# Optimization experiments

Hardware: AMD Instinct MI355X
Metric: run time of the kernel (lower is better)

## Reference

```python
import jax, jax.numpy as jnp
import numpy as np
from jax import lax

B, S, IN, H, HEAD, OUT = 256, 512, 64, 1024, 128, 64


def setup_inputs() -> dict:
    key = jax.random.key(0)
    ks = jax.random.split(key, 9)
    sc = 0.05
    return {
        "x": jax.random.normal(ks[0], (B, S, IN), jnp.float32),
        "W_ih": jax.random.normal(ks[1], (4 * H, IN), jnp.float32) * sc,
        "b_ih": jax.random.normal(ks[2], (4 * H,), jnp.float32) * sc,
        "W_hh": jax.random.normal(ks[3], (4 * H, H), jnp.float32) * sc,
        "b_hh": jax.random.normal(ks[4], (4 * H,), jnp.float32) * sc,
        "W_dense": jax.random.normal(ks[5], (HEAD, H), jnp.float32) * sc,
        "b_dense": jax.random.normal(ks[6], (HEAD,), jnp.float32) * sc,
        "W_dense2": jax.random.normal(ks[7], (OUT, HEAD), jnp.float32) * sc,
        "b_dense2": jax.random.normal(ks[8], (OUT,), jnp.float32) * sc,
    }


def reference(x, W_ih, b_ih, W_hh, b_hh, W_dense, b_dense, W_dense2, b_dense2):
    batch = x.shape[0]
    hid = W_hh.shape[1]
    # Precompute input-to-gate projections for all timesteps in one big GEMM.
    # x: [B,S,IN] -> xg: [S,B,4H]
    xg = jnp.einsum("bsi,gi->sbg", x, W_ih) + b_ih + b_hh

    def step(carry, xg_t):
        h, c = carry
        gates = xg_t + h @ W_hh.T  # [B,4H]; PyTorch LSTMCell gate order i,f,g,o
        i, f, g, o = jnp.split(gates, 4, axis=-1)
        c = jax.nn.sigmoid(f) * c + jax.nn.sigmoid(i) * jnp.tanh(g)
        h = jax.nn.sigmoid(o) * jnp.tanh(c)
        pred = jax.nn.relu(h @ W_dense.T + b_dense) @ W_dense2.T + b_dense2
        return (h, c), pred

    h0 = jnp.zeros((batch, hid), x.dtype)
    c0 = jnp.zeros((batch, hid), x.dtype)
    _, out = lax.scan(step, (h0, c0), xg)  # out: [S,B,OUT]
    return jnp.swapaxes(out, 0, 1)  # [B,S,OUT]
```

## Files before the change

### kernel.cpp

```cpp
#include <hip/hip_runtime.h>

typedef _Float16 half_t;
typedef _Float16 half8 __attribute__((ext_vector_type(8)));
typedef _Float16 half4 __attribute__((ext_vector_type(4)));
typedef float float4v __attribute__((ext_vector_type(4)));

#define BB    256
#define SS    512
#define IND   64
#define HH    1024
#define HEADD 128
#define OUTD  64
#define NKT   34
#define WLDS_HALVES (4 * NKT * 512)
#define PRE_STRIDE 68
#define DP_OFF   (WLDS_HALVES * 2 + 4 * 16 * PRE_STRIDE * 4)
#define FLAG_OFF (DP_OFF + 3 * 64 * 4 * 4)
#define SMEM_BYTES (FLAG_OFF + 32)
#define BUFV (BB * HH)
#define GO_OFF   8192
#define DCNT_OFF 10240
#define SYNC_WORDS 10368

#define MFMA16(a, b, acc) __builtin_amdgcn_mfma_f32_16x16x32_f16(a, b, acc, 0, 0, 0)

__device__ half_t g_hA[(size_t)(SS + 1) * BUFV];
__device__ half_t g_dbuf[(size_t)SS * 256 * HEADD];
__device__ unsigned int g_sync[SYNC_WORDS];

__device__ __forceinline__ void astore8(half_t* p, half4 v) {
  union { half4 h; unsigned long long u; } r; r.h = v;
  __hip_atomic_store((unsigned long long*)p, r.u, __ATOMIC_RELAXED,
                     __HIP_MEMORY_SCOPE_AGENT);
}
__device__ __forceinline__ void astore2(half_t* p, half_t v) {
  union { half_t h; unsigned short u; } r; r.h = v;
  __hip_atomic_store((unsigned short*)p, r.u, __ATOMIC_RELAXED,
                     __HIP_MEMORY_SCOPE_AGENT);
}


__global__ __launch_bounds__(256) void init_state() {
  const size_t i = (size_t)blockIdx.x * 256 + threadIdx.x;
  *(unsigned long long*)(g_hA + i * 4) = 0ULL;
  if (blockIdx.x == 0)
    for (int j = threadIdx.x; j < SYNC_WORDS; j += 256) g_sync[j] = 0;
}

__global__ __launch_bounds__(256) void pack_x(const float* __restrict__ x,
                                              half_t* __restrict__ xA) {
  const int t = blockIdx.x, mt = blockIdx.y;
  const int tid = threadIdx.x;
  const int kt = tid >> 7;
  const int lane = (tid >> 1) & 63;
  const int jh = (tid & 1) * 4;
  const int row = mt * 16 + (lane & 15);
  const int k = kt * 32 + (lane >> 4) * 8 + jh;
  const float* s = x + (size_t)row * SS * IND + (size_t)t * IND + k;
  half_t* d = xA + (((size_t)t * 16 + mt) * 2 + kt) * 512 + lane * 8 + jh;
  d[0] = (half_t)s[0]; d[1] = (half_t)s[1];
  d[2] = (half_t)s[2]; d[3] = (half_t)s[3];
}

__global__ __launch_bounds__(256) void frag_pack(const float* __restrict__ src,
                                                 half_t* __restrict__ dst, int K) {
  const int cb = blockIdx.x;
  const int tid = threadIdx.x;
  const int lane = tid & 63;
  const int u = tid >> 6;
  const int nkt = K >> 5;
  const int row = cb * 16 + (lane & 15);
  for (int kt = u; kt < nkt; kt += 4) {
    const int k = kt * 32 + (lane >> 4) * 8;
    const float* s = src + (size_t)row * K + k;
    half8 h;
    #pragma unroll
    for (int j = 0; j < 8; ++j) h[j] = (half_t)s[j];
    *(half8*)(dst + ((size_t)cb * nkt + kt) * 512 + lane * 8) = h;
  }
}

__global__ __launch_bounds__(512, 2) void lstm_persistent(
    const float* __restrict__ W_hh, const float* __restrict__ W_ih,
    const float* __restrict__ b_ih, const float* __restrict__ b_hh,
    const half_t* __restrict__ xA, const half_t* __restrict__ Wd_f,
    const float* __restrict__ bd, const half_t* __restrict__ Wd2_f,
    const float* __restrict__ bd2, float* __restrict__ out) {
  extern __shared__ char smem[];
  half_t* Wlds = (half_t*)smem;
  float* pre = (float*)(smem + (size_t)WLDS_HALVES * 2);
  float* dp = (float*)(smem + DP_OFF);
  unsigned* flg = (unsigned*)(smem + FLAG_OFF);

  const int bid = blockIdx.x;
  const int xcd = bid & 7;
  const int mtile = xcd >> 1;
  const int jtile = ((bid >> 3) << 1) | (xcd & 1);
  const int j0 = jtile * 16;
  const int tid = threadIdx.x;
  const int wave = tid >> 6;
  const int lane = tid & 63;
  const int rn = lane & 15;
  const int kq = lane >> 4;

  {
    const int g = wave & 3;
    const int row = g * HH + j0 + rn;
    for (int kt = (wave >> 2); kt < NKT; kt += 2) {
      const int k = kt * 32 + kq * 8;
      const float* s = (k < HH) ? (W_hh + (size_t)row * HH + k)
                                : (W_ih + (size_t)row * IND + (k - HH));
      half8 hv;
      #pragma unroll
      for (int j = 0; j < 8; ++j) hv[j] = (half_t)s[j];
      *(half8*)(Wlds + ((size_t)g * NKT + kt) * 512 + lane * 8) = hv;
    }
  }
  if (tid < 8) flg[tid] = 0;
  __syncthreads();

  unsigned short* slotp =
      (unsigned short*)(g_sync + ((size_t)(mtile * 64 + jtile)) * 32);
  unsigned int* go_base = g_sync + GO_OFF + mtile * 512;
  const unsigned int* gop = go_base + (jtile & 15) * 32;
  unsigned int* dcnt = g_sync + DCNT_OFF + mtile * 32;

  if (wave < 4) {
    const int crow = lane >> 2;
    const int hl = (lane & 3) * 4;
    float bsum[4][4];
    #pragma unroll
    for (int g = 0; g < 4; ++g) {
      const float4v bi = *(const float4v*)(b_ih + g * HH + j0 + hl);
      const float4v bh = *(const float4v*)(b_hh + g * HH + j0 + hl);
      #pragma unroll
      for (int j = 0; j < 4; ++j) bsum[g][j] = bi[j] + bh[j];
    }
    float4v creg = {0.f, 0.f, 0.f, 0.f};

    const int mtA = mtile * 4 + wave;
    float* pw = pre + wave * (16 * PRE_STRIDE);

    const int col_s = j0 + hl;
    const int ktw = col_s >> 5;
    const int kqw = (col_s & 31) >> 3;
    const int jw = col_s & 7;
    const size_t hoff =
        (((size_t)(mtA * 32 + ktw)) * 64 + kqw * 16 + crow) * 8 + jw;

    const half_t* habase = g_hA + ((size_t)mtA * 32) * 512 + lane * 8;
    const half_t* bp = Wlds + lane * 8;
    unsigned short* myslot = slotp + wave;

    half8 breg0[8], breg1[8], breg2[8], breg3[8];
    #pragma unroll
    for (int kt = 0; kt < 8; ++kt) {
      breg0[kt] = *(const half8*)(bp + (size_t)(0 * NKT + kt) * 512);
      breg1[kt] = *(const half8*)(bp + (size_t)(1 * NKT + kt) * 512);
      breg2[kt] = *(const half8*)(bp + (size_t)(2 * NKT + kt) * 512);
      breg3[kt] = *(const half8*)(bp + (size_t)(3 * NKT + kt) * 512);
    }

    for (int t = 0; t < SS; ++t) {
      float4v a0 = {0.f, 0.f, 0.f, 0.f}, a1 = {0.f, 0.f, 0.f, 0.f};
      float4v a2 = {0.f, 0.f, 0.f, 0.f}, a3 = {0.f, 0.f, 0.f, 0.f};

      const half_t* xp = xA + (((size_t)t * 16 + mtA) * 2) * 512 + lane * 8;
      {
        const half8 xv0 = *(const half8*)xp;
        const half8 xv1 = *(const half8*)(xp + 512);
        a0 = MFMA16(xv0, *(const half8*)(bp + (size_t)(0 * NKT + 32) * 512), a0);
        a1 = MFMA16(xv0, *(const half8*)(bp + (size_t)(1 * NKT + 32) * 512), a1);
        a2 = MFMA16(xv0, *(const half8*)(bp + (size_t)(2 * NKT + 32) * 512), a2);
        a3 = MFMA16(xv0, *(const half8*)(bp + (size_t)(3 * NKT + 32) * 512), a3);
        a0 = MFMA16(xv1, *(const half8*)(bp + (size_t)(0 * NKT + 33) * 512), a0);
        a1 = MFMA16(xv1, *(const half8*)(bp + (size_t)(1 * NKT + 33) * 512), a1);
        a2 = MFMA16(xv1, *(const half8*)(bp + (size_t)(2 * NKT + 33) * 512), a2);
        a3 = MFMA16(xv1, *(const half8*)(bp + (size_t)(3 * NKT + 33) * 512), a3);
      }

      if (t >= 1) {
        const unsigned tt = (unsigned)t;
        while (__hip_atomic_load(gop, __ATOMIC_RELAXED,
                                 __HIP_MEMORY_SCOPE_AGENT) < tt)
          __builtin_amdgcn_s_sleep(1);
        asm volatile("" ::: "memory");
        if (wave == 0 && lane == 0)
          __hip_atomic_store(&flg[3], tt, __ATOMIC_RELEASE,
                             __HIP_MEMORY_SCOPE_WORKGROUP);
      }

      const half_t* ap = habase + (size_t)t * BUFV;
      #pragma unroll
      for (int kt = 0; kt < 8; ++kt) {
        const half8 av = *(const half8*)(ap + (size_t)kt * 512);
        a0 = MFMA16(av, breg0[kt], a0);
        a1 = MFMA16(av, breg1[kt], a1);
        a2 = MFMA16(av, breg2[kt], a2);
        a3 = MFMA16(av, breg3[kt], a3);
      }
      #pragma unroll 8
      for (int kt = 8; kt < 32; ++kt) {
        const half8 av = *(const half8*)(ap + (size_t)kt * 512);
        a0 = MFMA16(av, *(const half8*)(bp + (size_t)(0 * NKT + kt) * 512), a0);
        a1 = MFMA16(av, *(const half8*)(bp + (size_t)(1 * NKT + kt) * 512), a1);
        a2 = MFMA16(av, *(const half8*)(bp + (size_t)(2 * NKT + kt) * 512), a2);
        a3 = MFMA16(av, *(const half8*)(bp + (size_t)(3 * NKT + kt) * 512), a3);
      }

      #pragma unroll
      for (int r = 0; r < 4; ++r) {
        const int rl = (kq * 4 + r) * PRE_STRIDE;
        pw[rl + rn] = a0[r];
        pw[rl + 16 + rn] = a1[r];
        pw[rl + 32 + rn] = a2[r];
        pw[rl + 48 + rn] = a3[r];
      }

      const float4v pg0 = *(const float4v*)(pw + crow * PRE_STRIDE + hl);
      const float4v pg1 = *(const float4v*)(pw + crow * PRE_STRIDE + 16 + hl);
      const float4v pg2 = *(const float4v*)(pw + crow * PRE_STRIDE + 32 + hl);
      const float4v pg3 = *(const float4v*)(pw + crow * PRE_STRIDE + 48 + hl);
      half4 hnew;
      #pragma unroll
      for (int jj = 0; jj < 4; ++jj) {
        const float ig = pg0[jj] + bsum[0][jj];
        const float fg = pg1[jj] + bsum[1][jj];
        const float gg = pg2[jj] + bsum[2][jj];
        const float og = pg3[jj] + bsum[3][jj];
        const float is = 1.f / (1.f + __expf(-ig));
        const float fs = 1.f / (1.f + __expf(-fg));
        const float os = 1.f / (1.f + __expf(-og));
        const float gt = tanhf(gg);
        const float cn = fs * creg[jj] + is * gt;
        creg[jj] = cn;
        hnew[jj] = (half_t)(os * tanhf(cn));
      }
      astore8(g_hA + (size_t)(t + 1) * BUFV + hoff, hnew);

      __builtin_amdgcn_s_waitcnt(0);
      if (lane == 0)
        __hip_atomic_store(myslot, (unsigned short)(t + 1), __ATOMIC_RELAXED,
                           __HIP_MEMORY_SCOPE_AGENT);
    }

    if (wave == 0) {
      while (__hip_atomic_load(gop, __ATOMIC_RELAXED,
                               __HIP_MEMORY_SCOPE_AGENT) < (unsigned)SS)
        __builtin_amdgcn_s_sleep(1);
      asm volatile("" ::: "memory");
      if (lane == 0)
        __hip_atomic_store(&flg[3], (unsigned)SS, __ATOMIC_RELEASE,
                           __HIP_MEMORY_SCOPE_WORKGROUP);
    }

  } else if (jtile < 32) {
    const int u = wave - 4;
    const int rb = jtile >> 3, cb = jtile & 7;
    const int mt = mtile * 4 + rb;
    const half_t* hb = g_hA + ((size_t)mt * 32 + u * 8) * 512 + lane * 8;
    const half_t* bb = Wd_f + ((size_t)cb * 32 + u * 8) * 512 + lane * 8;

    for (int s = 1; s <= SS; ++s) {
      while (__hip_atomic_load(&flg[3], __ATOMIC_ACQUIRE,
                               __HIP_MEMORY_SCOPE_WORKGROUP) < (unsigned)s)
        __builtin_amdgcn_s_sleep(2);
      asm volatile("" ::: "memory");

      const half_t* ap = hb + (size_t)s * BUFV;
      float4v acc = {0.f, 0.f, 0.f, 0.f};
      #pragma unroll
      for (int kt = 0; kt < 8; ++kt)
        acc = MFMA16(*(const half8*)(ap + (size_t)kt * 512),
                     *(const half8*)(bb + (size_t)kt * 512), acc);

      if (u) {
        if (s > 1)
          while (__hip_atomic_load(&flg[4], __ATOMIC_ACQUIRE,
                                   __HIP_MEMORY_SCOPE_WORKGROUP) <
                 (unsigned)(s - 1))
            __builtin_amdgcn_s_sleep(1);
        *(float4v*)(dp + ((size_t)(u - 1) * 64 + lane) * 4) = acc;
        __hip_atomic_store(&flg[u - 1], (unsigned)s, __ATOMIC_RELEASE,
                           __HIP_MEMORY_SCOPE_WORKGROUP);
      } else {
        for (;;) {
          const unsigned f0 = __hip_atomic_load(&flg[0], __ATOMIC_ACQUIRE,
                                                __HIP_MEMORY_SCOPE_WORKGROUP);
          const unsigned f1 = __hip_atomic_load(&flg[1], __ATOMIC_ACQUIRE,
                                                __HIP_MEMORY_SCOPE_WORKGROUP);
          const unsigned f2 = __hip_atomic_load(&flg[2], __ATOMIC_ACQUIRE,
                                                __HIP_MEMORY_SCOPE_WORKGROUP);
          if (f0 >= (unsigned)s && f1 >= (unsigned)s && f2 >= (unsigned)s) break;
          __builtin_amdgcn_s_sleep(1);
        }
        asm volatile("" ::: "memory");
        #pragma unroll
        for (int i = 0; i < 3; ++i) {
          const float4v p = *(const float4v*)(dp + ((size_t)i * 64 + lane) * 4);
          #pragma unroll
          for (int r = 0; r < 4; ++r) acc[r] += p[r];
        }
        __hip_atomic_store(&flg[4], (unsigned)s, __ATOMIC_RELEASE,
                           __HIP_MEMORY_SCOPE_WORKGROUP);
        const int dcol = cb * 16 + rn;
        const float bv = bd[dcol];
        half_t* db = g_dbuf + (((size_t)(s - 1) * 16 + mt) * 16) * HEADD + dcol;
        #pragma unroll
        for (int r = 0; r < 4; ++r)
          astore2(db + (size_t)(kq * 4 + r) * HEADD,
                  (half_t)fmaxf(acc[r] + bv, 0.f));
        __builtin_amdgcn_s_waitcnt(0);
        if (lane == 0)
          __hip_atomic_fetch_add(dcnt, 1u, __ATOMIC_RELAXED,
                                 __HIP_MEMORY_SCOPE_AGENT);
      }
    }

  } else if (jtile < 48 && wave == 4) {
    const int task = jtile - 32;
    const int rb = task >> 2, cb2 = task & 3;
    const int mt = mtile * 4 + rb;
    const int m0 = mtile * 64;
    const half_t* bp2 = Wd2_f + (size_t)cb2 * 4 * 512 + lane * 8;
    for (int d = 0; d < SS; ++d) {
      if (lane == 0) {
        const unsigned tgt = 32u * (unsigned)(d + 1);
        while (__hip_atomic_load(dcnt, __ATOMIC_RELAXED,
                                 __HIP_MEMORY_SCOPE_AGENT) < tgt)
          __builtin_amdgcn_s_sleep(16);
      }
      asm volatile("" ::: "memory");
      const half_t* ap = g_dbuf + (((size_t)d * 16 + mt) * 16) * HEADD;
      float4v acc = {0.f, 0.f, 0.f, 0.f};
      #pragma unroll
      for (int kt = 0; kt < 4; ++kt) {
        const half8 af =
            *(const half8*)(ap + (size_t)rn * HEADD + kt * 32 + kq * 8);
        acc = MFMA16(af, *(const half8*)(bp2 + (size_t)kt * 512), acc);
      }
      const int ocol = cb2 * 16 + rn;
      const float bv = bd2[ocol];
      #pragma unroll
      for (int r = 0; r < 4; ++r) {
        const int row = m0 + rb * 16 + kq * 4 + r;
        out[(size_t)row * (SS * OUTD) + (size_t)d * OUTD + ocol] = acc[r] + bv;
      }
    }

  } else if (jtile == 63 && wave == 5) {
    const unsigned long long* pollp =
        (const unsigned long long*)(g_sync + ((size_t)(mtile * 64 + lane)) * 32);
    for (int t = 1; t <= SS; ++t) {
      const unsigned tt = (unsigned)t;
      for (;;) {
        const unsigned long long v = __hip_atomic_load(
            pollp, __ATOMIC_RELAXED, __HIP_MEMORY_SCOPE_AGENT);
        const unsigned f0 = (unsigned)(v & 0xffffu);
        const unsigned f1 = (unsigned)((v >> 16) & 0xffffu);
        const unsigned f2 = (unsigned)((v >> 32) & 0xffffu);
        const unsigned f3 = (unsigned)(v >> 48);
        if (__all((int)(f0 >= tt && f1 >= tt && f2 >= tt && f3 >= tt))) break;
        __builtin_amdgcn_s_sleep(1);
      }
      asm volatile("" ::: "memory");
      if (lane < 16)
        __hip_atomic_store(go_base + lane * 32, tt, __ATOMIC_RELAXED,
                           __HIP_MEMORY_SCOPE_AGENT);
    }
  }
}

extern "C" void kernel_launch(void* const* d_in, const int* in_sizes, int n_in,
                              void* d_out, int out_size, void* d_ws, size_t ws_size,
                              hipStream_t stream) {
  const float* x        = (const float*)d_in[0];
  const float* W_ih     = (const float*)d_in[1];
  const float* b_ih     = (const float*)d_in[2];
  const float* W_hh     = (const float*)d_in[3];
  const float* b_hh     = (const float*)d_in[4];
  const float* W_dense  = (const float*)d_in[5];
  const float* b_dense  = (const float*)d_in[6];
  const float* W_dense2 = (const float*)d_in[7];
  const float* b_dense2 = (const float*)d_in[8];
  float* out = (float*)d_out;

  char* p = (char*)d_ws;
  half_t* xA    = (half_t*)p; p += (size_t)SS * 16 * 1024 * 2;
  half_t* Wd_f  = (half_t*)p; p += (size_t)8 * 32 * 512 * 2;
  half_t* Wd2_f = (half_t*)p; p += (size_t)4 * 4 * 512 * 2;

  init_state<<<256, 256, 0, stream>>>();
  pack_x<<<dim3(SS, 16), 256, 0, stream>>>(x, xA);
  frag_pack<<<HEADD / 16, 256, 0, stream>>>(W_dense, Wd_f, HH);
  frag_pack<<<OUTD / 16, 256, 0, stream>>>(W_dense2, Wd2_f, HEADD);

  hipFuncSetAttribute((const void*)lstm_persistent,
                      hipFuncAttributeMaxDynamicSharedMemorySize, SMEM_BYTES);
  void* args[] = {(void*)&W_hh, (void*)&W_ih, (void*)&b_ih, (void*)&b_hh,
                  (void*)&xA, (void*)&Wd_f, (void*)&b_dense,
                  (void*)&Wd2_f, (void*)&b_dense2, (void*)&out};
  hipLaunchCooperativeKernel((void*)lstm_persistent, dim3(256), dim3(512),
                             args, SMEM_BYTES, stream);
}
```

Before: 4.263 ms.

## Replace full hidden-state history with an 8-slot ring buffer and hoist dense weights

Stores the hidden state in an 8-entry ring buffer instead of a buffer holding every timestep, so the working set stays cache-resident instead of streaming 513 full hidden-state copies through memory. To stop slots being overwritten too early, the recurrent waves now wait on the dense-stage completion counter before reusing a slot, and acquire fences replace the compiler-only barriers. The dense-head and output-stage weight fragments are also hoisted into registers. In exchange the recurrence can stall on the dense consumers, and the extra registers may reduce occupancy or cause spills.

New measurement: 9.600 ms. 2.25x slower.

```diff
diff --git a/kernel.cpp b/kernel.cpp
--- a/kernel.cpp
+++ b/kernel.cpp
@@ -18,13 +18,14 @@
 #define FLAG_OFF (DP_OFF + 3 * 64 * 4 * 4)
 #define SMEM_BYTES (FLAG_OFF + 32)
 #define BUFV (BB * HH)
+#define HRING 8
 #define GO_OFF   8192
 #define DCNT_OFF 10240
 #define SYNC_WORDS 10368
 
 #define MFMA16(a, b, acc) __builtin_amdgcn_mfma_f32_16x16x32_f16(a, b, acc, 0, 0, 0)
 
-__device__ half_t g_hA[(size_t)(SS + 1) * BUFV];
+__device__ half_t g_hA[(size_t)HRING * BUFV];
 __device__ half_t g_dbuf[(size_t)SS * 256 * HEADD];
 __device__ unsigned int g_sync[SYNC_WORDS];
 
@@ -148,7 +149,7 @@
     const size_t hoff =
         (((size_t)(mtA * 32 + ktw)) * 64 + kqw * 16 + crow) * 8 + jw;
 
-    const half_t* habase = g_hA + ((size_t)mtA * 32) * 512 + lane * 8;
+    const size_t hbase_off = ((size_t)mtA * 32) * 512 + lane * 8;
     const half_t* bp = Wlds + lane * 8;
     unsigned short* myslot = slotp + wave;
 
@@ -162,6 +163,11 @@
     }
 
     for (int t = 0; t < SS; ++t) {
+      unsigned dc = 0;
+      if (t >= 8)
+        dc = __hip_atomic_load(dcnt, __ATOMIC_RELAXED,
+                               __HIP_MEMORY_SCOPE_AGENT);
+
       float4v a0 = {0.f, 0.f, 0.f, 0.f}, a1 = {0.f, 0.f, 0.f, 0.f};
       float4v a2 = {0.f, 0.f, 0.f, 0.f}, a3 = {0.f, 0.f, 0.f, 0.f};
 
@@ -184,13 +190,22 @@
         while (__hip_atomic_load(gop, __ATOMIC_RELAXED,
                                  __HIP_MEMORY_SCOPE_AGENT) < tt)
           __builtin_amdgcn_s_sleep(1);
-        asm volatile("" ::: "memory");
+        __builtin_amdgcn_fence(__ATOMIC_ACQUIRE, "agent");
         if (wave == 0 && lane == 0)
           __hip_atomic_store(&flg[3], tt, __ATOMIC_RELEASE,
                              __HIP_MEMORY_SCOPE_WORKGROUP);
       }
 
-      const half_t* ap = habase + (size_t)t * BUFV;
+      if (t >= 8) {
+        const unsigned need = 32u * (unsigned)(t - 7);
+        while (dc < need) {
+          __builtin_amdgcn_s_sleep(1);
+          dc = __hip_atomic_load(dcnt, __ATOMIC_RELAXED,
+                                 __HIP_MEMORY_SCOPE_AGENT);
+        }
+      }
+
+      const half_t* ap = g_hA + (size_t)(t & 7) * BUFV + hbase_off;
       #pragma unroll
       for (int kt = 0; kt < 8; ++kt) {
         const half8 av = *(const half8*)(ap + (size_t)kt * 512);
@@ -236,7 +251,7 @@
         creg[jj] = cn;
         hnew[jj] = (half_t)(os * tanhf(cn));
       }
-      astore8(g_hA + (size_t)(t + 1) * BUFV + hoff, hnew);
+      astore8(g_hA + (size_t)((t + 1) & 7) * BUFV + hoff, hnew);
 
       __builtin_amdgcn_s_waitcnt(0);
       if (lane == 0)
@@ -258,21 +273,25 @@
     const int u = wave - 4;
     const int rb = jtile >> 3, cb = jtile & 7;
     const int mt = mtile * 4 + rb;
-    const half_t* hb = g_hA + ((size_t)mt * 32 + u * 8) * 512 + lane * 8;
+    const size_t hb_off = ((size_t)mt * 32 + u * 8) * 512 + lane * 8;
     const half_t* bb = Wd_f + ((size_t)cb * 32 + u * 8) * 512 + lane * 8;
+
+    half8 bbreg[8];
+    #pragma unroll
+    for (int kt = 0; kt < 8; ++kt)
+      bbreg[kt] = *(const half8*)(bb + (size_t)kt * 512);
 
     for (int s = 1; s <= SS; ++s) {
       while (__hip_atomic_load(&flg[3], __ATOMIC_ACQUIRE,
                                __HIP_MEMORY_SCOPE_WORKGROUP) < (unsigned)s)
         __builtin_amdgcn_s_sleep(2);
-      asm volatile("" ::: "memory");
-
-      const half_t* ap = hb + (size_t)s * BUFV;
+      __builtin_amdgcn_fence(__ATOMIC_ACQUIRE, "agent");
+
+      const half_t* ap = g_hA + (size_t)(s & 7) * BUFV + hb_off;
       float4v acc = {0.f, 0.f, 0.f, 0.f};
       #pragma unroll
       for (int kt = 0; kt < 8; ++kt)
-        acc = MFMA16(*(const half8*)(ap + (size_t)kt * 512),
-                     *(const half8*)(bb + (size_t)kt * 512), acc);
+        acc = MFMA16(*(const half8*)(ap + (size_t)kt * 512), bbreg[kt], acc);
 
       if (u) {
         if (s > 1)
@@ -323,6 +342,10 @@
     const int mt = mtile * 4 + rb;
     const int m0 = mtile * 64;
     const half_t* bp2 = Wd2_f + (size_t)cb2 * 4 * 512 + lane * 8;
+    half8 b2reg[4];
+    #pragma unroll
+    for (int kt = 0; kt < 4; ++kt)
+      b2reg[kt] = *(const half8*)(bp2 + (size_t)kt * 512);
     for (int d = 0; d < SS; ++d) {
       if (lane == 0) {
         const unsigned tgt = 32u * (unsigned)(d + 1);
@@ -337,7 +360,7 @@
       for (int kt = 0; kt < 4; ++kt) {
         const half8 af =
             *(const half8*)(ap + (size_t)rn * HEADD + kt * 32 + kq * 8);
-        acc = MFMA16(af, *(const half8*)(bp2 + (size_t)kt * 512), acc);
+        acc = MFMA16(af, b2reg[kt], acc);
       }
       const int ocol = cb2 * 16 + rn;
       const float bv = bd2[ocol];
```

## Poll per-tile step slots directly in each block, dropping the central go-flag aggregator

Applied to the files above, without the earlier changes.

Removes the dedicated aggregator wave that polled all per-tile progress slots and then broadcast a go counter. Each recurrent block's wave 0 now polls the 64 slots itself and releases its sibling waves through a workgroup-scope LDS flag. This cuts one cross-CU hop from the per-timestep critical path, at the cost of many more blocks polling the same global slot lines. It also keeps the dense-head B fragments in registers instead of reloading them every step.

After: 4.431 ms. 1.04x slower.

```diff
diff --git a/kernel.cpp b/kernel.cpp
--- a/kernel.cpp
+++ b/kernel.cpp
@@ -18,7 +18,6 @@
 #define FLAG_OFF (DP_OFF + 3 * 64 * 4 * 4)
 #define SMEM_BYTES (FLAG_OFF + 32)
 #define BUFV (BB * HH)
-#define GO_OFF   8192
 #define DCNT_OFF 10240
 #define SYNC_WORDS 10368
 
@@ -121,8 +120,8 @@
 
   unsigned short* slotp =
       (unsigned short*)(g_sync + ((size_t)(mtile * 64 + jtile)) * 32);
-  unsigned int* go_base = g_sync + GO_OFF + mtile * 512;
-  const unsigned int* gop = go_base + (jtile & 15) * 32;
+  const unsigned long long* pollp =
+      (const unsigned long long*)(g_sync + ((size_t)(mtile * 64 + lane)) * 32);
   unsigned int* dcnt = g_sync + DCNT_OFF + mtile * 32;
 
   if (wave < 4) {
@@ -181,13 +180,28 @@
 
       if (t >= 1) {
         const unsigned tt = (unsigned)t;
-        while (__hip_atomic_load(gop, __ATOMIC_RELAXED,
-                                 __HIP_MEMORY_SCOPE_AGENT) < tt)
-          __builtin_amdgcn_s_sleep(1);
+        if (wave == 0) {
+          for (;;) {
+            const unsigned long long v = __hip_atomic_load(
+                pollp, __ATOMIC_RELAXED, __HIP_MEMORY_SCOPE_AGENT);
+            const unsigned f0 = (unsigned)(v & 0xffffu);
+            const unsigned f1 = (unsigned)((v >> 16) & 0xffffu);
+            const unsigned f2 = (unsigned)((v >> 32) & 0xffffu);
+            const unsigned f3 = (unsigned)(v >> 48);
+            if (__all((int)(f0 >= tt && f1 >= tt && f2 >= tt && f3 >= tt)))
+              break;
+            __builtin_amdgcn_s_sleep(1);
+          }
+          asm volatile("" ::: "memory");
+          if (lane == 0)
+            __hip_atomic_store(&flg[3], tt, __ATOMIC_RELEASE,
+                               __HIP_MEMORY_SCOPE_WORKGROUP);
+        } else {
+          while (__hip_atomic_load(&flg[3], __ATOMIC_ACQUIRE,
+                                   __HIP_MEMORY_SCOPE_WORKGROUP) < tt)
+            __builtin_amdgcn_s_sleep(1);
+        }
         asm volatile("" ::: "memory");
-        if (wave == 0 && lane == 0)
-          __hip_atomic_store(&flg[3], tt, __ATOMIC_RELEASE,
-                             __HIP_MEMORY_SCOPE_WORKGROUP);
       }
 
       const half_t* ap = habase + (size_t)t * BUFV;
@@ -245,12 +259,20 @@
     }
 
     if (wave == 0) {
-      while (__hip_atomic_load(gop, __ATOMIC_RELAXED,
-                               __HIP_MEMORY_SCOPE_AGENT) < (unsigned)SS)
+      const unsigned tt = (unsigned)SS;
+      for (;;) {
+        const unsigned long long v = __hip_atomic_load(
+            pollp, __ATOMIC_RELAXED, __HIP_MEMORY_SCOPE_AGENT);
+        const unsigned f0 = (unsigned)(v & 0xffffu);
+        const unsigned f1 = (unsigned)((v >> 16) & 0xffffu);
+        const unsigned f2 = (unsigned)((v >> 32) & 0xffffu);
+        const unsigned f3 = (unsigned)(v >> 48);
+        if (__all((int)(f0 >= tt && f1 >= tt && f2 >= tt && f3 >= tt))) break;
         __builtin_amdgcn_s_sleep(1);
+      }
       asm volatile("" ::: "memory");
       if (lane == 0)
-        __hip_atomic_store(&flg[3], (unsigned)SS, __ATOMIC_RELEASE,
+        __hip_atomic_store(&flg[3], tt, __ATOMIC_RELEASE,
                            __HIP_MEMORY_SCOPE_WORKGROUP);
     }
 
@@ -261,6 +283,11 @@
     const half_t* hb = g_hA + ((size_t)mt * 32 + u * 8) * 512 + lane * 8;
     const half_t* bb = Wd_f + ((size_t)cb * 32 + u * 8) * 512 + lane * 8;
 
+    half8 bbreg[8];
+    #pragma unroll
+    for (int kt = 0; kt < 8; ++kt)
+      bbreg[kt] = *(const half8*)(bb + (size_t)kt * 512);
+
     for (int s = 1; s <= SS; ++s) {
       while (__hip_atomic_load(&flg[3], __ATOMIC_ACQUIRE,
                                __HIP_MEMORY_SCOPE_WORKGROUP) < (unsigned)s)
@@ -271,8 +298,7 @@
       float4v acc = {0.f, 0.f, 0.f, 0.f};
       #pragma unroll
       for (int kt = 0; kt < 8; ++kt)
-        acc = MFMA16(*(const half8*)(ap + (size_t)kt * 512),
-                     *(const half8*)(bb + (size_t)kt * 512), acc);
+        acc = MFMA16(*(const half8*)(ap + (size_t)kt * 512), bbreg[kt], acc);
 
       if (u) {
         if (s > 1)
@@ -323,6 +349,10 @@
     const int mt = mtile * 4 + rb;
     const int m0 = mtile * 64;
     const half_t* bp2 = Wd2_f + (size_t)cb2 * 4 * 512 + lane * 8;
+    half8 b2reg[4];
+    #pragma unroll
+    for (int kt = 0; kt < 4; ++kt)
+      b2reg[kt] = *(const half8*)(bp2 + (size_t)kt * 512);
     for (int d = 0; d < SS; ++d) {
       if (lane == 0) {
         const unsigned tgt = 32u * (unsigned)(d + 1);
@@ -337,7 +367,7 @@
       for (int kt = 0; kt < 4; ++kt) {
         const half8 af =
             *(const half8*)(ap + (size_t)rn * HEADD + kt * 32 + kq * 8);
-        acc = MFMA16(af, *(const half8*)(bp2 + (size_t)kt * 512), acc);
+        acc = MFMA16(af, b2reg[kt], acc);
       }
       const int ocol = cb2 * 16 + rn;
       const float bv = bd2[ocol];
@@ -346,27 +376,6 @@
         const int row = m0 + rb * 16 + kq * 4 + r;
         out[(size_t)row * (SS * OUTD) + (size_t)d * OUTD + ocol] = acc[r] + bv;
       }
-    }
-
-  } else if (jtile == 63 && wave == 5) {
-    const unsigned long long* pollp =
-        (const unsigned long long*)(g_sync + ((size_t)(mtile * 64 + lane)) * 32);
-    for (int t = 1; t <= SS; ++t) {
-      const unsigned tt = (unsigned)t;
-      for (;;) {
-        const unsigned long long v = __hip_atomic_load(
-            pollp, __ATOMIC_RELAXED, __HIP_MEMORY_SCOPE_AGENT);
-        const unsigned f0 = (unsigned)(v & 0xffffu);
-        const unsigned f1 = (unsigned)((v >> 16) & 0xffffu);
-        const unsigned f2 = (unsigned)((v >> 32) & 0xffffu);
-        const unsigned f3 = (unsigned)(v >> 48);
-        if (__all((int)(f0 >= tt && f1 >= tt && f2 >= tt && f3 >= tt))) break;
-        __builtin_amdgcn_s_sleep(1);
-      }
-      asm volatile("" ::: "memory");
-      if (lane < 16)
-        __hip_atomic_store(go_base + lane * 32, tt, __ATOMIC_RELAXED,
-                           __HIP_MEMORY_SCOPE_AGENT);
     }
   }
 }
```
